# Kernel optimization log

Measured on AMD Instinct MI355X. Metric: run time of the kernel, lower is better.

The kernel has to match this reference:

```python
import jax, jax.numpy as jnp
import numpy as np

B, S, HID, H, DH = 8, 4096, 1024, 16, 64


def setup_inputs() -> dict:
    key = jax.random.key(0)
    ks = jax.random.split(key, 5)
    return {
        "hidden_states": jax.random.normal(ks[0], (B, S, HID), dtype=jnp.float32),
        "attention_mask": jnp.ones((B, 1, 1, S), dtype=jnp.float32),
        "Wq": jax.random.normal(ks[1], (HID, HID), dtype=jnp.float32) * (HID ** -0.5),
        "Wk": jax.random.normal(ks[2], (HID, HID), dtype=jnp.float32) * (HID ** -0.5),
        "Wv": jax.random.normal(ks[3], (HID, HID), dtype=jnp.float32) * (HID ** -0.5),
        "att_weight": jax.random.normal(ks[4], (H, 1, DH), dtype=jnp.float32) * (DH ** -0.5),
    }


def _heads(x):
    # [B,S,HID] -> [B,H,S,DH]
    b, s, _ = x.shape
    return x.reshape(b, s, H, DH).transpose(0, 2, 1, 3)


def reference(hidden_states, attention_mask, Wq, Wk, Wv, att_weight):
    # bias-free projections (torch Linear: x @ W.T)
    q = _heads(hidden_states @ Wq.T)  # [B,H,S,DH]
    k = _heads(hidden_states @ Wk.T)
    v = _heads(hidden_states @ Wv.T)

    mask = attention_mask.transpose(0, 1, 3, 2)  # [B,1,S,1]
    aw = att_weight[:, 0, :]  # [H,DH]

    q_scores = jnp.einsum('bhsd,hd->bhs', q, aw)[..., None] * mask  # [B,H,S,1]
    k_scores = jnp.einsum('bhsd,hd->bhs', k, aw)[..., None] * mask  # [B,H,S,1]

    length = jnp.sum(mask, axis=-2, keepdims=True)            # [B,1,1,1]
    mean_value = jnp.sum(v * mask, axis=-2, keepdims=True)    # [B,H,1,DH]

    query_values = q_scores * mean_value                      # [B,H,S,DH] outer product
    key_values = jnp.einsum('bhs,bhsd->bhd', k_scores[..., 0], v)[:, :, None, :]  # [B,H,1,DH]

    ctx = (query_values + key_values) / length                # [B,H,S,DH]
    ctx = ctx.transpose(0, 2, 1, 3).reshape(ctx.shape[0], ctx.shape[2], H * DH)
    return ctx
```

## Files before the change

kernel.cpp:

```cpp
#include <hip/hip_runtime.h>

#define BB 8
#define SS 4096
#define HIDD 1024
#define HH 16
#define DHH 64

__global__ __launch_bounds__(256) void k_prep(const float* __restrict__ Wq,
                                              const float* __restrict__ Wk,
                                              const float* __restrict__ aw,
                                              float* __restrict__ wq_f,
                                              float* __restrict__ wk_f) {
    int i = blockIdx.x * 256 + threadIdx.x;
    int h = blockIdx.y;
    const float* W = blockIdx.z ? Wk : Wq;
    float* outp = blockIdx.z ? wk_f : wq_f;
    float acc = 0.f;
#pragma unroll
    for (int d = 0; d < DHH; ++d) {
        acc += aw[h * DHH + d] * W[(size_t)(h * DHH + d) * HIDD + i];
    }
    outp[h * HIDD + i] = acc;
}

#define KC 128
#define LSTR 129
__global__ __launch_bounds__(256, 4) void k_scores(const float* __restrict__ hid,
                                                   const float* __restrict__ mask,
                                                   const float* __restrict__ weff,
                                                   float* __restrict__ qsb,
                                                   float* __restrict__ ksb) {
    __shared__ float sh[64 * LSTR];

    const int t    = threadIdx.x;
    const int wave = t >> 6;
    const int lane = t & 63;
    const int obase = __builtin_amdgcn_readfirstlane(blockIdx.x * 16 + wave * 4);

    const int row  = blockIdx.y * 64 + lane;
    const size_t gbase = (size_t)blockIdx.y * 64 * HIDD;

    float acc[4] = {0.f, 0.f, 0.f, 0.f};

    float4 stg[8];
#pragma unroll
    for (int j = 0; j < 8; ++j) {
        int f  = j * 256 + t;
        int r  = f >> 5;
        int c4 = f & 31;
        stg[j] = *reinterpret_cast<const float4*>(
            hid + gbase + (size_t)r * HIDD + c4 * 4);
    }

    for (int chunk = 0; chunk < HIDD / KC; ++chunk) {
        __syncthreads();
#pragma unroll
        for (int j = 0; j < 8; ++j) {
            int f  = j * 256 + t;
            int r  = f >> 5;
            int c4 = f & 31;
            float* d = sh + r * LSTR + c4 * 4;
            d[0] = stg[j].x; d[1] = stg[j].y; d[2] = stg[j].z; d[3] = stg[j].w;
        }
        __syncthreads();
        if (chunk + 1 < HIDD / KC) {
#pragma unroll
            for (int j = 0; j < 8; ++j) {
                int f  = j * 256 + t;
                int r  = f >> 5;
                int c4 = f & 31;
                stg[j] = *reinterpret_cast<const float4*>(
                    hid + gbase + (size_t)r * HIDD + (chunk + 1) * KC + c4 * 4);
            }
        }

        const float* wc = weff + chunk * KC;
#pragma unroll 8
        for (int k = 0; k < KC; k += 4) {
            float h0 = sh[lane * LSTR + k];
            float h1 = sh[lane * LSTR + k + 1];
            float h2 = sh[lane * LSTR + k + 2];
            float h3 = sh[lane * LSTR + k + 3];
#pragma unroll
            for (int o = 0; o < 4; ++o) {
                float4 wv = *reinterpret_cast<const float4*>(
                    wc + (size_t)(obase + o) * HIDD + k);
                acc[o] += h0 * wv.x + h1 * wv.y + h2 * wv.z + h3 * wv.w;
            }
        }
    }

    float m = mask[row];
#pragma unroll
    for (int o = 0; o < 4; ++o) acc[o] *= m;

    float4 v = make_float4(acc[0], acc[1], acc[2], acc[3]);
    if (blockIdx.x == 0) {
        *reinterpret_cast<float4*>(qsb + (size_t)row * 16 + obase) = v;
    } else {
        *reinterpret_cast<float4*>(ksb + (size_t)row * 20 + (obase - 16)) = v;
        if (obase == 16) ksb[(size_t)row * 20 + 16] = m;
    }
}

__global__ __launch_bounds__(256) void k_ksh(const float* __restrict__ hid,
                                             const float* __restrict__ ksb,
                                             float* __restrict__ part) {
    int b  = blockIdx.z;
    int i  = blockIdx.y * 512 + threadIdx.x * 2;
    int s0 = blockIdx.x * 128;

    float acc0[17], acc1[17];
#pragma unroll
    for (int c = 0; c < 17; ++c) { acc0[c] = 0.f; acc1[c] = 0.f; }

    const float* hb = hid + (size_t)(b * SS + s0) * HIDD + i;
    const float* sb = ksb + (size_t)(b * SS + s0) * 20;

#pragma unroll 8
    for (int s = 0; s < 128; ++s) {
        float2 hv = *reinterpret_cast<const float2*>(hb + (size_t)s * HIDD);
        const float* sc = sb + s * 20;
#pragma unroll
        for (int c = 0; c < 17; ++c) {
            float scv = sc[c];
            acc0[c] += scv * hv.x;
            acc1[c] += scv * hv.y;
        }
    }

    float* pb = part + (((size_t)blockIdx.x * 8 + b) * 17) * 1024 + i;
#pragma unroll
    for (int c = 0; c < 17; ++c) {
        *reinterpret_cast<float2*>(pb + c * 1024) = make_float2(acc0[c], acc1[c]);
    }
}

__global__ __launch_bounds__(256) void k_red(const float* __restrict__ part,
                                             float* __restrict__ ksh,
                                             float* __restrict__ hsum) {
    int gid = blockIdx.x * 256 + threadIdx.x;
    int b = gid / 17408;
    int r = gid - b * 17408;
    int c = r >> 10;
    int i = r & 1023;

    float s = 0.f;
#pragma unroll 8
    for (int k = 0; k < 32; ++k)
        s += part[(((size_t)k * 8 + b) * 17 + c) * 1024 + i];

    if (c < 16) ksh[((size_t)b * 16 + c) * 1024 + i] = s;
    else        hsum[b * 1024 + i] = s;
}

__global__ __launch_bounds__(256) void k_fin(const float* __restrict__ Wv,
                                             const float* __restrict__ mask,
                                             const float* __restrict__ hsum,
                                             const float* __restrict__ ksh,
                                             float* __restrict__ mvn,
                                             float* __restrict__ kvn) {
    int b  = blockIdx.x;
    int j  = blockIdx.y * 32 + (threadIdx.x >> 3);
    int sl = threadIdx.x & 7;

    __shared__ float red[256];
    float lsum = 0.f;
    for (int s = threadIdx.x; s < SS; s += 256) lsum += mask[b * SS + s];
    red[threadIdx.x] = lsum;
    __syncthreads();
    for (int off = 128; off; off >>= 1) {
        if (threadIdx.x < off) red[threadIdx.x] += red[threadIdx.x + off];
        __syncthreads();
    }
    float invlen = 1.0f / red[0];

    int h = j >> 6;
    const float4* w4 = reinterpret_cast<const float4*>(Wv + (size_t)j * HIDD + sl * 128);
    const float4* hv = reinterpret_cast<const float4*>(hsum + b * HIDD + sl * 128);
    const float4* kv = reinterpret_cast<const float4*>(ksh + ((size_t)b * 16 + h) * HIDD + sl * 128);

    float mv = 0.f, kvv = 0.f;
#pragma unroll
    for (int c = 0; c < 32; ++c) {
        float4 w = w4[c], a = hv[c], k2 = kv[c];
        mv  += w.x * a.x  + w.y * a.y  + w.z * a.z  + w.w * a.w;
        kvv += w.x * k2.x + w.y * k2.y + w.z * k2.z + w.w * k2.w;
    }
#pragma unroll
    for (int off = 1; off < 8; off <<= 1) {
        mv  += __shfl_xor(mv, off);
        kvv += __shfl_xor(kvv, off);
    }
    if (sl == 0) {
        mvn[b * HIDD + j] = mv * invlen;
        kvn[b * HIDD + j] = kvv * invlen;
    }
}

__global__ __launch_bounds__(256) void k_out(const float* __restrict__ qsb,
                                             const float* __restrict__ mvn,
                                             const float* __restrict__ kvn,
                                             float* __restrict__ outp) {
    size_t e0 = ((size_t)blockIdx.x * 256 + threadIdx.x) * 8;
    int b   = (int)(e0 >> 22);
    int rem = (int)(e0 & ((1u << 22) - 1));
    int s   = rem >> 10;
    int j   = rem & 1023;

    float q = qsb[(size_t)(b * SS + s) * 16 + (j >> 6)];
    const float4* mv4 = reinterpret_cast<const float4*>(mvn + b * HIDD + j);
    const float4* kv4 = reinterpret_cast<const float4*>(kvn + b * HIDD + j);
    float4 m0 = mv4[0], m1 = mv4[1];
    float4 k0 = kv4[0], k1 = kv4[1];

    float4 o0, o1;
    o0.x = q * m0.x + k0.x;  o0.y = q * m0.y + k0.y;
    o0.z = q * m0.z + k0.z;  o0.w = q * m0.w + k0.w;
    o1.x = q * m1.x + k1.x;  o1.y = q * m1.y + k1.y;
    o1.z = q * m1.z + k1.z;  o1.w = q * m1.w + k1.w;

    float4* op = reinterpret_cast<float4*>(outp + e0);
    op[0] = o0;
    op[1] = o1;
}

extern "C" void kernel_launch(void* const* d_in, const int* in_sizes, int n_in,
                              void* d_out, int out_size, void* d_ws, size_t ws_size,
                              hipStream_t stream) {
    const float* hid  = (const float*)d_in[0];
    const float* mask = (const float*)d_in[1];
    const float* Wq   = (const float*)d_in[2];
    const float* Wk   = (const float*)d_in[3];
    const float* Wv   = (const float*)d_in[4];
    const float* aw   = (const float*)d_in[5];
    float* outp = (float*)d_out;

    float* ws   = (float*)d_ws;
    float* wq_f = ws;
    float* wk_f = wq_f + 16384;
    float* qsb  = wk_f + 16384;
    float* ksb  = qsb + 524288;
    float* ksh  = ksb + 655360;
    float* hsum = ksh + 131072;
    float* mvn  = hsum + 8192;
    float* kvn  = mvn + 8192;
    float* part = kvn + 8192;

    k_prep  <<<dim3(4, 16, 2), 256, 0, stream>>>(Wq, Wk, aw, wq_f, wk_f);
    k_scores<<<dim3(2, 512),   256, 0, stream>>>(hid, mask, wq_f, qsb, ksb);
    k_ksh   <<<dim3(32, 2, 8), 256, 0, stream>>>(hid, ksb, part);
    k_red   <<<dim3(544),      256, 0, stream>>>(part, ksh, hsum);
    k_fin   <<<dim3(8, 32),    256, 0, stream>>>(Wv, mask, hsum, ksh, mvn, kvn);
    k_out   <<<dim3(16384),    256, 0, stream>>>(qsb, mvn, kvn, outp);
}
```

Baseline: 332.5 us.

## Merge q/k score blocks and widen per-thread work in score and ksh kernels

k_scores now has each block compute all 32 output score columns (q and k) for its 64 rows, so the hidden-state tile is loaded from global memory once instead of twice. The LDS stride is padded to 132 so rows can be written and read as float4. k_ksh processes four hidden columns per thread over 64-row slabs with one block per batch slab, and k_red sums 64 partials instead of 32. In exchange, per-thread register use rises (8 accumulators and 17 float4 accumulators), and float4 LDS reads at a 132-float stride may cause bank conflicts.

```diff
diff --git a/kernel.cpp b/kernel.cpp
--- a/kernel.cpp
+++ b/kernel.cpp
@@ -24,7 +24,7 @@
 }
 
 #define KC 128
-#define LSTR 129
+#define LSTR 132
 __global__ __launch_bounds__(256, 4) void k_scores(const float* __restrict__ hid,
                                                    const float* __restrict__ mask,
                                                    const float* __restrict__ weff,
@@ -35,12 +35,14 @@
     const int t    = threadIdx.x;
     const int wave = t >> 6;
     const int lane = t & 63;
-    const int obase = __builtin_amdgcn_readfirstlane(blockIdx.x * 16 + wave * 4);
-
-    const int row  = blockIdx.y * 64 + lane;
-    const size_t gbase = (size_t)blockIdx.y * 64 * HIDD;
-
-    float acc[4] = {0.f, 0.f, 0.f, 0.f};
+    const int obase = __builtin_amdgcn_readfirstlane(wave * 8);
+
+    const int row  = blockIdx.x * 64 + lane;
+    const size_t gbase = (size_t)blockIdx.x * 64 * HIDD;
+
+    float acc[8];
+#pragma unroll
+    for (int o = 0; o < 8; ++o) acc[o] = 0.f;
 
     float4 stg[8];
 #pragma unroll
@@ -59,8 +61,7 @@
             int f  = j * 256 + t;
             int r  = f >> 5;
             int c4 = f & 31;
-            float* d = sh + r * LSTR + c4 * 4;
-            d[0] = stg[j].x; d[1] = stg[j].y; d[2] = stg[j].z; d[3] = stg[j].w;
+            *reinterpret_cast<float4*>(sh + r * LSTR + c4 * 4) = stg[j];
         }
         __syncthreads();
         if (chunk + 1 < HIDD / KC) {
@@ -77,28 +78,28 @@
         const float* wc = weff + chunk * KC;
 #pragma unroll 8
         for (int k = 0; k < KC; k += 4) {
-            float h0 = sh[lane * LSTR + k];
-            float h1 = sh[lane * LSTR + k + 1];
-            float h2 = sh[lane * LSTR + k + 2];
-            float h3 = sh[lane * LSTR + k + 3];
-#pragma unroll
-            for (int o = 0; o < 4; ++o) {
+            float4 h4 = *reinterpret_cast<const float4*>(sh + lane * LSTR + k);
+#pragma unroll
+            for (int o = 0; o < 8; ++o) {
                 float4 wv = *reinterpret_cast<const float4*>(
                     wc + (size_t)(obase + o) * HIDD + k);
-                acc[o] += h0 * wv.x + h1 * wv.y + h2 * wv.z + h3 * wv.w;
+                acc[o] += h4.x * wv.x + h4.y * wv.y + h4.z * wv.z + h4.w * wv.w;
             }
         }
     }
 
     float m = mask[row];
 #pragma unroll
-    for (int o = 0; o < 4; ++o) acc[o] *= m;
-
-    float4 v = make_float4(acc[0], acc[1], acc[2], acc[3]);
-    if (blockIdx.x == 0) {
-        *reinterpret_cast<float4*>(qsb + (size_t)row * 16 + obase) = v;
+    for (int o = 0; o < 8; ++o) acc[o] *= m;
+
+    float4 v0 = make_float4(acc[0], acc[1], acc[2], acc[3]);
+    float4 v1 = make_float4(acc[4], acc[5], acc[6], acc[7]);
+    if (obase < 16) {
+        float4* p = reinterpret_cast<float4*>(qsb + (size_t)row * 16 + obase);
+        p[0] = v0; p[1] = v1;
     } else {
-        *reinterpret_cast<float4*>(ksb + (size_t)row * 20 + (obase - 16)) = v;
+        float4* p = reinterpret_cast<float4*>(ksb + (size_t)row * 20 + (obase - 16));
+        p[0] = v0; p[1] = v1;
         if (obase == 16) ksb[(size_t)row * 20 + 16] = m;
     }
 }
@@ -106,33 +107,35 @@
 __global__ __launch_bounds__(256) void k_ksh(const float* __restrict__ hid,
                                              const float* __restrict__ ksb,
                                              float* __restrict__ part) {
-    int b  = blockIdx.z;
-    int i  = blockIdx.y * 512 + threadIdx.x * 2;
-    int s0 = blockIdx.x * 128;
-
-    float acc0[17], acc1[17];
-#pragma unroll
-    for (int c = 0; c < 17; ++c) { acc0[c] = 0.f; acc1[c] = 0.f; }
+    int b  = blockIdx.y;
+    int i  = threadIdx.x * 4;
+    int s0 = blockIdx.x * 64;
+
+    float4 acc[17];
+#pragma unroll
+    for (int c = 0; c < 17; ++c) acc[c] = make_float4(0.f, 0.f, 0.f, 0.f);
 
     const float* hb = hid + (size_t)(b * SS + s0) * HIDD + i;
     const float* sb = ksb + (size_t)(b * SS + s0) * 20;
 
-#pragma unroll 8
-    for (int s = 0; s < 128; ++s) {
-        float2 hv = *reinterpret_cast<const float2*>(hb + (size_t)s * HIDD);
+#pragma unroll 4
+    for (int s = 0; s < 64; ++s) {
+        float4 hv = *reinterpret_cast<const float4*>(hb + (size_t)s * HIDD);
         const float* sc = sb + s * 20;
 #pragma unroll
         for (int c = 0; c < 17; ++c) {
             float scv = sc[c];
-            acc0[c] += scv * hv.x;
-            acc1[c] += scv * hv.y;
+            acc[c].x += scv * hv.x;
+            acc[c].y += scv * hv.y;
+            acc[c].z += scv * hv.z;
+            acc[c].w += scv * hv.w;
         }
     }
 
     float* pb = part + (((size_t)blockIdx.x * 8 + b) * 17) * 1024 + i;
 #pragma unroll
     for (int c = 0; c < 17; ++c) {
-        *reinterpret_cast<float2*>(pb + c * 1024) = make_float2(acc0[c], acc1[c]);
+        *reinterpret_cast<float4*>(pb + c * 1024) = acc[c];
     }
 }
 
@@ -147,7 +150,7 @@
 
     float s = 0.f;
 #pragma unroll 8
-    for (int k = 0; k < 32; ++k)
+    for (int k = 0; k < 64; ++k)
         s += part[(((size_t)k * 8 + b) * 17 + c) * 1024 + i];
 
     if (c < 16) ksh[((size_t)b * 16 + c) * 1024 + i] = s;
@@ -248,8 +251,8 @@
     float* part = kvn + 8192;
 
     k_prep  <<<dim3(4, 16, 2), 256, 0, stream>>>(Wq, Wk, aw, wq_f, wk_f);
-    k_scores<<<dim3(2, 512),   256, 0, stream>>>(hid, mask, wq_f, qsb, ksb);
-    k_ksh   <<<dim3(32, 2, 8), 256, 0, stream>>>(hid, ksb, part);
+    k_scores<<<dim3(512),      256, 0, stream>>>(hid, mask, wq_f, qsb, ksb);
+    k_ksh   <<<dim3(64, 8),    256, 0, stream>>>(hid, ksb, part);
     k_red   <<<dim3(544),      256, 0, stream>>>(part, ksh, hsum);
     k_fin   <<<dim3(8, 32),    256, 0, stream>>>(Wv, mask, hsum, ksh, mvn, kvn);
     k_out   <<<dim3(16384),    256, 0, stream>>>(qsb, mvn, kvn, outp);
```

Result: slower. 428.7 us (+28.9%).
